# Performance work log

Measured on AMD Instinct MI355X. Metric: run time of the kernel, lower is better.

Reference implementation:

```python
import jax, jax.numpy as jnp
import numpy as np

B, N, NAB, NF, NG = 2, 512, 128, 128, 32
CUTOFF = 5.0


def ssp(x):
    # shifted softplus: ln(1+e^x) - ln 2
    return jax.nn.softplus(x) - jnp.log(2.0).astype(x.dtype)


def setup_inputs() -> dict:
    key = jax.random.key(0)
    ks = jax.random.split(key, 10)
    offsets = jnp.linspace(0.0, CUTOFF, NG)
    widths = jnp.full((NG,), offsets[1] - offsets[0])
    s = 0.05
    return {
        "r": jax.random.normal(ks[0], (B, N, NAB), jnp.float32),
        "e": jax.random.uniform(ks[1], (B, N, N), jnp.float32),
        "A": jax.random.uniform(ks[2], (B, N, N), jnp.float32),
        "offsets": offsets,
        "widths": widths,
        "W_df1": jax.random.normal(ks[3], (NG, NG), jnp.float32) * s,
        "b_df1": jnp.zeros((NG,), jnp.float32),
        "W_df2": jax.random.normal(ks[4], (NG, NF), jnp.float32) * s,
        "b_df2": jnp.zeros((NF,), jnp.float32),
        "W_af": jax.random.normal(ks[5], (NAB, NF), jnp.float32) * s,
        "W_d1": jax.random.normal(ks[6], (NF, NAB), jnp.float32) * s,
        "b_d1": jnp.zeros((NAB,), jnp.float32),
        "W_d2": jax.random.normal(ks[7], (NAB, NAB), jnp.float32) * s,
        "b_d2": jnp.zeros((NAB,), jnp.float32),
    }


def reference(r, e, A, offsets, widths, W_df1, b_df1, W_df2, b_df2,
              W_af, W_d1, b_d1, W_d2, b_d2):
    # Gaussian smearing (trainable offsets/widths, non-centered)
    coeff = -0.5 / (widths ** 2)                       # [G]
    diff = e[:, :, :, None] - offsets[None, None, None, :]  # [B,N,N,G]
    es = jnp.exp(coeff * diff ** 2)                    # [B,N,N,G]
    # DistanceFilter1 output is computed then discarded (faithful to source)
    _ = ssp(es @ W_df1 + b_df1)
    W = es @ W_df2 + b_df2                             # [B,N,N,F]
    rf = r @ W_af                                      # [B,N,F]
    # cfconv: broadcast-multiply-reduce over neighbor axis j
    y = jnp.einsum("bjf,bij,bijf->bif", rf, A, W)      # [B,N,F]
    y = ssp(y @ W_d1 + b_d1)                           # [B,N,NAB]
    y = y @ W_d2 + b_d2                                # [B,N,NAB]
    return y
```

## Files before the change

### kernel.cpp

```cpp
#include <hip/hip_runtime.h>
#include <math.h>

#define BB 2
#define NN 512
#define NAB 128
#define NF 128
#define NG 32

typedef _Float16 f16;
typedef f16 f16x8 __attribute__((ext_vector_type(8)));
typedef f16 f16x4 __attribute__((ext_vector_type(4)));
typedef float f32x4 __attribute__((ext_vector_type(4)));

#define TS 520
#define SS 132

__global__ __launch_bounds__(256) void prep_rf(const float* __restrict__ r,
                                               const float* __restrict__ W_af,
                                               f16* __restrict__ rfT) {
    const int tid = threadIdx.x;
    const int r0  = blockIdx.x * 4;
    const int b   = r0 >> 9;
    const int j0  = r0 & 511;

    __shared__ float sr[4][128];
    __shared__ f16   st[128][8];

    for (int t = tid; t < 512; t += 256)
        sr[t >> 7][t & 127] = r[(r0 + (t >> 7)) * NAB + (t & 127)];
    __syncthreads();

    const int f  = tid & 127;
    const int rh = tid >> 7;
    float a0 = 0.f, a1 = 0.f;
    #pragma unroll 8
    for (int k = 0; k < NAB; ++k) {
        const float wv = W_af[k * NF + f];
        a0 += sr[2 * rh + 0][k] * wv;
        a1 += sr[2 * rh + 1][k] * wv;
    }
    st[f][2 * rh + 0] = (f16)a0;
    st[f][2 * rh + 1] = (f16)a1;
    __syncthreads();

    if (tid < 128) {
        f16x4 v;
        v[0] = st[tid][0]; v[1] = st[tid][1]; v[2] = st[tid][2]; v[3] = st[tid][3];
        *(f16x4*)(rfT + b * (NF * NN) + tid * NN + j0) = v;
    }
}

__global__ __launch_bounds__(256) void fused_kernel(
    const float* __restrict__ e, const float* __restrict__ A,
    const f16*  __restrict__ rfT,
    const float* __restrict__ offsets, const float* __restrict__ widths,
    const float* __restrict__ W_df2, const float* __restrict__ b_df2,
    const float* __restrict__ W_d1,  const float* __restrict__ b_d1,
    const float* __restrict__ W_d2,  const float* __restrict__ b_d2,
    float* __restrict__ out) {

    const int bi  = blockIdx.x;
    const int b   = bi >> 9;
    const int tid = threadIdx.x;
    const int w    = tid >> 6;
    const int lane = tid & 63;
    const int q    = lane >> 4;
    const int n    = lane & 15;

    __shared__ __align__(16) f16 Tsh[48 * TS];
    __shared__ float sconst[64];
    __shared__ float sy[128];
    __shared__ float spart[2][128];

    if (tid < NG) {
        sconst[tid] = offsets[tid];
        const float wd = widths[tid];
        sconst[32 + tid] = -0.5f / (wd * wd);
    }
    __syncthreads();

    for (int jj = tid; jj < NN; jj += 256) {
        const float ev = e[bi * NN + jj];
        const float av = A[bi * NN + jj];
        #pragma unroll
        for (int g = 0; g < NG; ++g) {
            const float d = ev - sconst[g];
            Tsh[g * TS + jj] = (f16)(av * __expf(sconst[32 + g] * d * d));
        }
        Tsh[32 * TS + jj] = (f16)av;
    }
    __syncthreads();

    f32x4 acc[3][2];
    #pragma unroll
    for (int mt = 0; mt < 3; ++mt)
        #pragma unroll
        for (int nt = 0; nt < 2; ++nt)
            acc[mt][nt] = (f32x4){0.f, 0.f, 0.f, 0.f};

    const f16* Ab = Tsh + n * TS + q * 8;
    const f16* Bb = rfT + (size_t)b * (NF * NN) + (w * 32 + n) * NN + q * 8;

    #pragma unroll 4
    for (int k = 0; k < NN; k += 32) {
        const f16x8 a0 = *(const f16x8*)(Ab + k);
        const f16x8 a1 = *(const f16x8*)(Ab + 16 * TS + k);
        const f16x8 a2 = *(const f16x8*)(Ab + 32 * TS + k);
        const f16x8 b0 = *(const f16x8*)(Bb + k);
        const f16x8 b1 = *(const f16x8*)(Bb + 16 * NN + k);
        acc[0][0] = __builtin_amdgcn_mfma_f32_16x16x32_f16(a0, b0, acc[0][0], 0, 0, 0);
        acc[1][0] = __builtin_amdgcn_mfma_f32_16x16x32_f16(a1, b0, acc[1][0], 0, 0, 0);
        acc[2][0] = __builtin_amdgcn_mfma_f32_16x16x32_f16(a2, b0, acc[2][0], 0, 0, 0);
        acc[0][1] = __builtin_amdgcn_mfma_f32_16x16x32_f16(a0, b1, acc[0][1], 0, 0, 0);
        acc[1][1] = __builtin_amdgcn_mfma_f32_16x16x32_f16(a1, b1, acc[1][1], 0, 0, 0);
        acc[2][1] = __builtin_amdgcn_mfma_f32_16x16x32_f16(a2, b1, acc[2][1], 0, 0, 0);
    }

    __syncthreads();
    float* S = (float*)Tsh;
    #pragma unroll
    for (int mt = 0; mt < 3; ++mt)
        #pragma unroll
        for (int nt = 0; nt < 2; ++nt)
            #pragma unroll
            for (int rr = 0; rr < 4; ++rr)
                S[(mt * 16 + q * 4 + rr) * SS + (w * 32 + nt * 16 + n)] = acc[mt][nt][rr];
    __syncthreads();

    if (tid < NF) {
        const int f = tid;
        float a = b_df2[f] * S[32 * SS + f];
        #pragma unroll 8
        for (int g = 0; g < NG; ++g)
            a += W_df2[g * NF + f] * S[g * SS + f];
        sy[f] = a;
    }
    __syncthreads();

    {
        const int f = tid & 127, hh = tid >> 7;
        float a = 0.f;
        #pragma unroll 8
        for (int k = hh * 64; k < hh * 64 + 64; ++k)
            a += sy[k] * W_d1[k * NAB + f];
        spart[hh][f] = a;
    }
    __syncthreads();
    float hreg = 0.f;
    if (tid < NAB) {
        const float x = spart[0][tid] + spart[1][tid] + b_d1[tid];
        const float sp = (x > 0.f) ? (x + log1pf(__expf(-x))) : log1pf(__expf(x));
        hreg = sp - 0.69314718055994530942f;
    }
    __syncthreads();
    if (tid < NAB) sy[tid] = hreg;
    __syncthreads();

    {
        const int f = tid & 127, hh = tid >> 7;
        float a = 0.f;
        #pragma unroll 8
        for (int k = hh * 64; k < hh * 64 + 64; ++k)
            a += sy[k] * W_d2[k * NAB + f];
        spart[hh][f] = a;
    }
    __syncthreads();
    if (tid < NAB)
        out[bi * NAB + tid] = spart[0][tid] + spart[1][tid] + b_d2[tid];
}

extern "C" void kernel_launch(void* const* d_in, const int* in_sizes, int n_in,
                              void* d_out, int out_size, void* d_ws, size_t ws_size,
                              hipStream_t stream) {
    const float* r       = (const float*)d_in[0];
    const float* e       = (const float*)d_in[1];
    const float* A       = (const float*)d_in[2];
    const float* offsets = (const float*)d_in[3];
    const float* widths  = (const float*)d_in[4];
    const float* W_df2   = (const float*)d_in[7];
    const float* b_df2   = (const float*)d_in[8];
    const float* W_af    = (const float*)d_in[9];
    const float* W_d1    = (const float*)d_in[10];
    const float* b_d1    = (const float*)d_in[11];
    const float* W_d2    = (const float*)d_in[12];
    const float* b_d2    = (const float*)d_in[13];
    float* out = (float*)d_out;

    f16* rfT = (f16*)d_ws;

    prep_rf<<<BB * NN / 4, 256, 0, stream>>>(r, W_af, rfT);
    fused_kernel<<<BB * NN, 256, 0, stream>>>(e, A, rfT, offsets, widths,
                                              W_df2, b_df2, W_d1, b_d1,
                                              W_d2, b_d2, out);
}
```

Measured before the change: 120.7 us.

## Split MFMA K-loop across waves, vectorize smearing, prefetch B, parallelize W_df2 reduce

The Gaussian smearing now has each thread load float4 chunks of e and A and write f16x4 vectors. Each thread covers four neighbours and half of the Gaussian bins. The MFMA loop is reorganised so the four waves split the K dimension in halves and the N dimension in 64-column halves, with a 3x4 accumulator tile per wave. The B operand from global memory is register double-buffered, and the two K-half partial sums are combined through LDS in two synchronized phases. The W_df2 contraction is split across all 256 threads, which costs extra LDS traffic and barriers.

New measurement: 116.0 us. 3.8% less time.

```diff
diff --git a/kernel.cpp b/kernel.cpp
--- a/kernel.cpp
+++ b/kernel.cpp
@@ -77,64 +77,124 @@
         const float wd = widths[tid];
         sconst[32 + tid] = -0.5f / (wd * wd);
     }
-    __syncthreads();
-
-    for (int jj = tid; jj < NN; jj += 256) {
-        const float ev = e[bi * NN + jj];
-        const float av = A[bi * NN + jj];
-        #pragma unroll
-        for (int g = 0; g < NG; ++g) {
-            const float d = ev - sconst[g];
-            Tsh[g * TS + jj] = (f16)(av * __expf(sconst[32 + g] * d * d));
-        }
-        Tsh[32 * TS + jj] = (f16)av;
-    }
-    __syncthreads();
-
-    f32x4 acc[3][2];
+
+    const int j0 = (tid & 127) * 4;
+    const float4 ev = *(const float4*)(e + bi * NN + j0);
+    const float4 av = *(const float4*)(A + bi * NN + j0);
+    __syncthreads();
+
+    #pragma unroll
+    for (int i = 0; i < 16; ++i) {
+        const int g = (tid >> 7) + 2 * i;
+        const float off = sconst[g];
+        const float cf  = sconst[32 + g];
+        const float d0 = ev.x - off, d1 = ev.y - off;
+        const float d2 = ev.z - off, d3 = ev.w - off;
+        f16x4 v;
+        v[0] = (f16)(av.x * __expf(cf * d0 * d0));
+        v[1] = (f16)(av.y * __expf(cf * d1 * d1));
+        v[2] = (f16)(av.z * __expf(cf * d2 * d2));
+        v[3] = (f16)(av.w * __expf(cf * d3 * d3));
+        *(f16x4*)(Tsh + g * TS + j0) = v;
+    }
+    if (tid < 128) {
+        f16x4 v;
+        v[0] = (f16)av.x; v[1] = (f16)av.y; v[2] = (f16)av.z; v[3] = (f16)av.w;
+        *(f16x4*)(Tsh + 32 * TS + j0) = v;
+    }
+    __syncthreads();
+
+    const int kh = w >> 1;
+    const int nh = w & 1;
+
+    f32x4 acc[3][4];
     #pragma unroll
     for (int mt = 0; mt < 3; ++mt)
         #pragma unroll
-        for (int nt = 0; nt < 2; ++nt)
+        for (int nt = 0; nt < 4; ++nt)
             acc[mt][nt] = (f32x4){0.f, 0.f, 0.f, 0.f};
 
-    const f16* Ab = Tsh + n * TS + q * 8;
-    const f16* Bb = rfT + (size_t)b * (NF * NN) + (w * 32 + n) * NN + q * 8;
-
-    #pragma unroll 4
-    for (int k = 0; k < NN; k += 32) {
-        const f16x8 a0 = *(const f16x8*)(Ab + k);
-        const f16x8 a1 = *(const f16x8*)(Ab + 16 * TS + k);
-        const f16x8 a2 = *(const f16x8*)(Ab + 32 * TS + k);
-        const f16x8 b0 = *(const f16x8*)(Bb + k);
-        const f16x8 b1 = *(const f16x8*)(Bb + 16 * NN + k);
-        acc[0][0] = __builtin_amdgcn_mfma_f32_16x16x32_f16(a0, b0, acc[0][0], 0, 0, 0);
-        acc[1][0] = __builtin_amdgcn_mfma_f32_16x16x32_f16(a1, b0, acc[1][0], 0, 0, 0);
-        acc[2][0] = __builtin_amdgcn_mfma_f32_16x16x32_f16(a2, b0, acc[2][0], 0, 0, 0);
-        acc[0][1] = __builtin_amdgcn_mfma_f32_16x16x32_f16(a0, b1, acc[0][1], 0, 0, 0);
-        acc[1][1] = __builtin_amdgcn_mfma_f32_16x16x32_f16(a1, b1, acc[1][1], 0, 0, 0);
-        acc[2][1] = __builtin_amdgcn_mfma_f32_16x16x32_f16(a2, b1, acc[2][1], 0, 0, 0);
+    const f16* Abase = Tsh + n * TS + kh * 256 + q * 8;
+    const f16* Bbase = rfT + (size_t)b * (NF * NN) + (nh * 64 + n) * NN + kh * 256 + q * 8;
+
+    f16x8 bcur[4], bnext[4];
+    #pragma unroll
+    for (int nt = 0; nt < 4; ++nt)
+        bcur[nt] = *(const f16x8*)(Bbase + nt * 16 * NN);
+
+    #pragma unroll
+    for (int kk = 0; kk < 8; ++kk) {
+        const f16* Ak = Abase + kk * 32;
+        const f16x8 a0 = *(const f16x8*)(Ak);
+        const f16x8 a1 = *(const f16x8*)(Ak + 16 * TS);
+        const f16x8 a2 = *(const f16x8*)(Ak + 32 * TS);
+        if (kk < 7) {
+            #pragma unroll
+            for (int nt = 0; nt < 4; ++nt)
+                bnext[nt] = *(const f16x8*)(Bbase + (kk + 1) * 32 + nt * 16 * NN);
+        }
+        #pragma unroll
+        for (int nt = 0; nt < 4; ++nt) {
+            acc[0][nt] = __builtin_amdgcn_mfma_f32_16x16x32_f16(a0, bcur[nt], acc[0][nt], 0, 0, 0);
+            acc[1][nt] = __builtin_amdgcn_mfma_f32_16x16x32_f16(a1, bcur[nt], acc[1][nt], 0, 0, 0);
+            acc[2][nt] = __builtin_amdgcn_mfma_f32_16x16x32_f16(a2, bcur[nt], acc[2][nt], 0, 0, 0);
+        }
+        #pragma unroll
+        for (int nt = 0; nt < 4; ++nt) bcur[nt] = bnext[nt];
     }
 
     __syncthreads();
     float* S = (float*)Tsh;
-    #pragma unroll
-    for (int mt = 0; mt < 3; ++mt)
-        #pragma unroll
-        for (int nt = 0; nt < 2; ++nt)
-            #pragma unroll
-            for (int rr = 0; rr < 4; ++rr)
-                S[(mt * 16 + q * 4 + rr) * SS + (w * 32 + nt * 16 + n)] = acc[mt][nt][rr];
-    __syncthreads();
-
-    if (tid < NF) {
-        const int f = tid;
-        float a = b_df2[f] * S[32 * SS + f];
-        #pragma unroll 8
-        for (int g = 0; g < NG; ++g)
-            a += W_df2[g * NF + f] * S[g * SS + f];
-        sy[f] = a;
-    }
+
+    if (kh == 0) {
+        #pragma unroll
+        for (int mt = 0; mt < 2; ++mt)
+            #pragma unroll
+            for (int nt = 0; nt < 4; ++nt)
+                #pragma unroll
+                for (int rr = 0; rr < 4; ++rr)
+                    S[(mt * 16 + q * 4 + rr) * SS + nh * 64 + nt * 16 + n] = acc[mt][nt][rr];
+        if (q == 0) {
+            #pragma unroll
+            for (int nt = 0; nt < 4; ++nt)
+                S[32 * SS + nh * 64 + nt * 16 + n] = acc[2][nt][0];
+        }
+    }
+    __syncthreads();
+    if (kh == 1) {
+        #pragma unroll
+        for (int mt = 0; mt < 2; ++mt)
+            #pragma unroll
+            for (int nt = 0; nt < 4; ++nt)
+                #pragma unroll
+                for (int rr = 0; rr < 4; ++rr)
+                    S[(mt * 16 + q * 4 + rr) * SS + nh * 64 + nt * 16 + n] += acc[mt][nt][rr];
+        if (q == 0) {
+            #pragma unroll
+            for (int nt = 0; nt < 4; ++nt)
+                S[32 * SS + nh * 64 + nt * 16 + n] += acc[2][nt][0];
+        }
+    }
+    __syncthreads();
+
+    {
+        const int f = tid & 127;
+        float a;
+        if (tid < 128) {
+            a = b_df2[f] * S[32 * SS + f];
+            #pragma unroll
+            for (int g = 0; g < 16; ++g)
+                a += W_df2[g * NF + f] * S[g * SS + f];
+        } else {
+            a = 0.f;
+            #pragma unroll
+            for (int g = 16; g < 32; ++g)
+                a += W_df2[g * NF + f] * S[g * SS + f];
+        }
+        spart[tid >> 7][f] = a;
+    }
+    __syncthreads();
+    if (tid < 128) sy[tid] = spart[0][tid] + spart[1][tid];
     __syncthreads();
 
     {
```
